# Kernel tuning notes

Measured on AMD Instinct MI355X. Metric: run time of the kernel, lower is better.

## Reference

```python
import jax, jax.numpy as jnp
import numpy as np

D_MODEL, N_HEADS, D_K, D_V = 1024, 16, 64, 64


def setup_inputs() -> dict:
    key = jax.random.key(0)
    ks = jax.random.split(key, 9)
    B, S = 8, 1024
    Q = jax.random.normal(ks[0], (B, S, D_MODEL), dtype=jnp.float32)
    K = jax.random.normal(ks[1], (B, S, D_MODEL), dtype=jnp.float32)
    V = jax.random.normal(ks[2], (B, S, D_MODEL), dtype=jnp.float32)
    # Xavier-uniform weights (gain=1): limit = sqrt(6/(fan_in+fan_out))
    lim = float(np.sqrt(6.0 / (D_MODEL + N_HEADS * D_K)))
    Wq = jax.random.uniform(ks[3], (D_MODEL, N_HEADS * D_K), minval=-lim, maxval=lim, dtype=jnp.float32)
    Wk = jax.random.uniform(ks[4], (D_MODEL, N_HEADS * D_K), minval=-lim, maxval=lim, dtype=jnp.float32)
    Wv = jax.random.uniform(ks[5], (D_MODEL, N_HEADS * D_V), minval=-lim, maxval=lim, dtype=jnp.float32)
    # nn.Linear default bias init: uniform(-1/sqrt(fan_in), 1/sqrt(fan_in))
    bl = float(1.0 / np.sqrt(D_MODEL))
    bq = jax.random.uniform(ks[6], (N_HEADS * D_K,), minval=-bl, maxval=bl, dtype=jnp.float32)
    bk = jax.random.uniform(ks[7], (N_HEADS * D_K,), minval=-bl, maxval=bl, dtype=jnp.float32)
    bv = jax.random.uniform(ks[8], (N_HEADS * D_V,), minval=-bl, maxval=bl, dtype=jnp.float32)
    return {"Q": Q, "K": K, "V": V, "Wq": Wq, "bq": bq, "Wk": Wk, "bk": bk, "Wv": Wv, "bv": bv}


def reference(Q, K, V, Wq, bq, Wk, bk, Wv, bv):
    B, S, _ = Q.shape
    # projections -> [B, H, S, d]
    q = (Q @ Wq + bq).reshape(B, S, N_HEADS, D_K).transpose(0, 2, 1, 3)
    k = (K @ Wk + bk).reshape(B, S, N_HEADS, D_K).transpose(0, 2, 1, 3)
    v = (V @ Wv + bv).reshape(B, S, N_HEADS, D_V).transpose(0, 2, 1, 3)
    scores = jnp.exp(jnp.einsum('bhqd,bhkd->bhqk', q, k) / jnp.sqrt(jnp.float32(D_K)))
    attn = scores / (jnp.sum(scores, axis=-1, keepdims=True) + 1e-8)
    ctx = jnp.einsum('bhqk,bhkd->bhqd', attn, v)  # [B,H,S,Dv]
    return ctx.transpose(0, 2, 1, 3).reshape(B, S, N_HEADS * D_V)
```

## Files before the change

### kernel.cpp

```cpp
#include <hip/hip_runtime.h>
#include <stdint.h>

#define DM 1024
#define HEADS 16
#define BATCH 8
#define SEQ 1024
#define MTOT 8192

typedef _Float16 half8 __attribute__((ext_vector_type(8)));
typedef _Float16 half4 __attribute__((ext_vector_type(4)));
typedef float floatx4 __attribute__((ext_vector_type(4)));

__device__ __forceinline__ void glds16(const void* g, void* l) {
    __builtin_amdgcn_global_load_lds(
        (const __attribute__((address_space(1))) void*)g,
        (__attribute__((address_space(3))) void*)l, 16, 0, 0);
}

__global__ __launch_bounds__(256) void cvt_inputs(
        const float* __restrict__ Q, const float* __restrict__ K,
        const float* __restrict__ V,
        _Float16* __restrict__ qb, _Float16* __restrict__ kb, _Float16* __restrict__ vb) {
    const float* src = blockIdx.y == 0 ? Q : (blockIdx.y == 1 ? K : V);
    _Float16* dst    = blockIdx.y == 0 ? qb : (blockIdx.y == 1 ? kb : vb);
    size_t i = ((size_t)blockIdx.x * 256 + threadIdx.x) * 8;
    float4 a = *(const float4*)(src + i);
    float4 b = *(const float4*)(src + i + 4);
    half8 h;
    h[0] = (_Float16)a.x; h[1] = (_Float16)a.y; h[2] = (_Float16)a.z; h[3] = (_Float16)a.w;
    h[4] = (_Float16)b.x; h[5] = (_Float16)b.y; h[6] = (_Float16)b.z; h[7] = (_Float16)b.w;
    *(half8*)(dst + i) = h;
}

__global__ __launch_bounds__(256) void cvt_w(
        const float* __restrict__ Wq, const float* __restrict__ Wk,
        const float* __restrict__ Wv,
        _Float16* __restrict__ wqt, _Float16* __restrict__ wkt, _Float16* __restrict__ wvt) {
    __shared__ float t[32][33];
    int z = blockIdx.z;
    const float* W = z == 0 ? Wq : (z == 1 ? Wk : Wv);
    _Float16* Wt   = z == 0 ? wqt : (z == 1 ? wkt : wvt);
    int k0 = blockIdx.x * 32, n0 = blockIdx.y * 32;
    int tx = threadIdx.x, ty = threadIdx.y;
#pragma unroll
    for (int i = 0; i < 4; i++)
        t[ty + i * 8][tx] = W[(size_t)(k0 + ty + i * 8) * DM + n0 + tx];
    __syncthreads();
#pragma unroll
    for (int i = 0; i < 4; i++)
        Wt[(size_t)(n0 + ty + i * 8) * DM + k0 + tx] = (_Float16)t[tx][ty + i * 8];
}

__global__ __launch_bounds__(256) void proj_gemm(
        const _Float16* __restrict__ qb, const _Float16* __restrict__ kb,
        const _Float16* __restrict__ vb,
        const _Float16* __restrict__ wqt, const _Float16* __restrict__ wkt,
        const _Float16* __restrict__ wvt,
        const float* __restrict__ bq, const float* __restrict__ bk,
        const float* __restrict__ bv,
        _Float16* __restrict__ qh, _Float16* __restrict__ kh, _Float16* __restrict__ vT) {
    __shared__ _Float16 As[128 * 64];
    __shared__ _Float16 Bs[128 * 64];
    int z = blockIdx.z;
    const _Float16* A  = z == 0 ? qb : (z == 1 ? kb : vb);
    const _Float16* Bw = z == 0 ? wqt : (z == 1 ? wkt : wvt);
    const float* bias  = z == 0 ? bq : (z == 1 ? bk : bv);
    int m0 = blockIdx.x * 128, n0 = blockIdx.y * 128;
    int tid = threadIdx.x, wid = tid >> 6, lane = tid & 63;
    int l15 = lane & 15, quad = lane >> 4;
    int wm = wid >> 1, wn = wid & 1;
    bool swapped = (z < 2);

    floatx4 acc[4][4] = {};

    for (int kb_ = 0; kb_ < 16; kb_++) {
        __syncthreads();
        int k0 = kb_ * 64;
        int r = (wid * 4) * 8 + (lane >> 3);
        int pg = (lane & 7) ^ (lane >> 3);
#pragma unroll
        for (int ii = 0; ii < 4; ii++) {
            int issue = wid * 4 + ii;
            int rr = r + ii * 8;
            glds16(A  + (size_t)(m0 + rr) * DM + k0 + pg * 8, &As[issue * 512]);
            glds16(Bw + (size_t)(n0 + rr) * DM + k0 + pg * 8, &Bs[issue * 512]);
        }
        __syncthreads();
#pragma unroll
        for (int kc = 0; kc < 2; kc++) {
            half8 a[4], b[4];
#pragma unroll
            for (int mt = 0; mt < 4; mt++) {
                int row = wm * 64 + mt * 16 + l15;
                int pl = (kc * 4 + quad) ^ (l15 & 7);
                a[mt] = *(const half8*)&As[row * 64 + pl * 8];
            }
#pragma unroll
            for (int nt = 0; nt < 4; nt++) {
                int row = wn * 64 + nt * 16 + l15;
                int pl = (kc * 4 + quad) ^ (l15 & 7);
                b[nt] = *(const half8*)&Bs[row * 64 + pl * 8];
            }
            if (swapped) {
#pragma unroll
                for (int mt = 0; mt < 4; mt++)
#pragma unroll
                    for (int nt = 0; nt < 4; nt++)
                        acc[mt][nt] = __builtin_amdgcn_mfma_f32_16x16x32_f16(
                            b[nt], a[mt], acc[mt][nt], 0, 0, 0);
            } else {
#pragma unroll
                for (int mt = 0; mt < 4; mt++)
#pragma unroll
                    for (int nt = 0; nt < 4; nt++)
                        acc[mt][nt] = __builtin_amdgcn_mfma_f32_16x16x32_f16(
                            a[mt], b[nt], acc[mt][nt], 0, 0, 0);
            }
        }
    }

    if (swapped) {
        float sc = (z == 0) ? 0.125f : 1.0f;
        _Float16* out = (z == 0) ? qh : kh;
#pragma unroll
        for (int nt = 0; nt < 4; nt++) {
            int d0 = n0 + wn * 64 + nt * 16 + quad * 4;
            int hh = d0 >> 6, dd = d0 & 63;
            floatx4 b4 = *(const floatx4*)&bias[d0];
#pragma unroll
            for (int mt = 0; mt < 4; mt++) {
                int s = m0 + wm * 64 + mt * 16 + l15;
                int b_ = s >> 10, ss = s & 1023;
                size_t off = ((size_t)(b_ * HEADS + hh)) * 65536 + (size_t)ss * 64 + dd;
                half4 hv;
#pragma unroll
                for (int r = 0; r < 4; r++)
                    hv[r] = (_Float16)((acc[mt][nt][r] + b4[r]) * sc);
                *(half4*)&out[off] = hv;
            }
        }
    } else {
#pragma unroll
        for (int nt = 0; nt < 4; nt++) {
            int d = n0 + wn * 64 + nt * 16 + l15;
            int hh = d >> 6, dd = d & 63;
            float bv_ = bias[d];
#pragma unroll
            for (int mt = 0; mt < 4; mt++) {
                int s0 = m0 + wm * 64 + mt * 16 + quad * 4;
                int b_ = s0 >> 10, ss = s0 & 1023;
                size_t off = ((size_t)(b_ * HEADS + hh)) * 65536 + (size_t)dd * 1024 + ss;
                half4 hv;
#pragma unroll
                for (int r = 0; r < 4; r++)
                    hv[r] = (_Float16)(acc[mt][nt][r] + bv_);
                *(half4*)&vT[off] = hv;
            }
        }
    }
}

__global__ __launch_bounds__(256) void attn(
        const _Float16* __restrict__ qh, const _Float16* __restrict__ kh,
        const _Float16* __restrict__ vT, float* __restrict__ out) {
    __shared__ _Float16 Ks[4096];
    __shared__ _Float16 Vs[4096];
    __shared__ _Float16 QP[16384];
    int qt = blockIdx.x, h = blockIdx.y, b = blockIdx.z;
    size_t base = ((size_t)(b * HEADS + h)) * 65536;
    int tid = threadIdx.x, wid = tid >> 6, lane = tid & 63;
    int l15 = lane & 15, quad = lane >> 4;
    int rs = lane >> 3;
    int pg = (lane & 7) ^ rs;

#pragma unroll
    for (int ii = 0; ii < 8; ii++) {
        int issue = wid * 8 + ii;
        int r = issue * 8 + rs;
        glds16(qh + base + (size_t)(qt * 256 + r) * 64 + pg * 8, &QP[issue * 512]);
    }
    __syncthreads();
    half8 qf[4][2];
#pragma unroll
    for (int mt = 0; mt < 4; mt++)
#pragma unroll
        for (int kc = 0; kc < 2; kc++) {
            int row = wid * 64 + mt * 16 + l15;
            int pl = (kc * 4 + quad) ^ (l15 & 7);
            qf[mt][kc] = *(const half8*)&QP[row * 64 + pl * 8];
        }
    __syncthreads();

    floatx4 oacc[4][4] = {};
    float rden[4] = {0.f, 0.f, 0.f, 0.f};
    _Float16* Pw = &QP[wid * 4096];

    for (int kt = 0; kt < 16; kt++) {
        __syncthreads();
#pragma unroll
        for (int ii = 0; ii < 2; ii++) {
            int issue = wid * 2 + ii;
            int r = issue * 8 + rs;
            glds16(kh + base + (size_t)(kt * 64 + r) * 64 + pg * 8, &Ks[issue * 512]);
            glds16(vT + base + (size_t)r * 1024 + kt * 64 + pg * 8, &Vs[issue * 512]);
        }
        __syncthreads();

#pragma unroll
        for (int hf = 0; hf < 2; hf++) {
            floatx4 sacc[2][4] = {};
#pragma unroll
            for (int kc = 0; kc < 2; kc++) {
                half8 kf[2];
#pragma unroll
                for (int kn2 = 0; kn2 < 2; kn2++) {
                    int kn = hf * 2 + kn2;
                    int pl = (kc * 4 + quad) ^ (l15 & 7);
                    kf[kn2] = *(const half8*)&Ks[(kn * 16 + l15) * 64 + pl * 8];
                }
#pragma unroll
                for (int kn2 = 0; kn2 < 2; kn2++)
#pragma unroll
                    for (int mt = 0; mt < 4; mt++)
                        sacc[kn2][mt] = __builtin_amdgcn_mfma_f32_16x16x32_f16(
                            kf[kn2], qf[mt][kc], sacc[kn2][mt], 0, 0, 0);
            }
#pragma unroll
            for (int kn2 = 0; kn2 < 2; kn2++) {
                int kn = hf * 2 + kn2;
#pragma unroll
                for (int mt = 0; mt < 4; mt++) {
                    half4 ph;
#pragma unroll
                    for (int r = 0; r < 4; r++) {
                        float p = __expf(sacc[kn2][mt][r]);
                        rden[mt] += p;
                        ph[r] = (_Float16)p;
                    }
                    *(half4*)&Pw[(kn * 2 + (quad >> 1)) * 512 + (mt * 16 + l15) * 8 +
                                 (quad & 1) * 4] = ph;
                }
            }
            half8 af[4], vf[4];
#pragma unroll
            for (int mt = 0; mt < 4; mt++)
                af[mt] = *(const half8*)&Pw[(hf * 4 + quad) * 512 + (mt * 16 + l15) * 8];
#pragma unroll
            for (int dn = 0; dn < 4; dn++) {
                int pl = (hf * 4 + quad) ^ (l15 & 7);
                vf[dn] = *(const half8*)&Vs[(dn * 16 + l15) * 64 + pl * 8];
            }
#pragma unroll
            for (int mt = 0; mt < 4; mt++)
#pragma unroll
                for (int dn = 0; dn < 4; dn++)
                    oacc[mt][dn] = __builtin_amdgcn_mfma_f32_16x16x32_f16(
                        af[mt], vf[dn], oacc[mt][dn], 0, 0, 0);
        }
    }

#pragma unroll
    for (int mt = 0; mt < 4; mt++) {
        float d = rden[mt];
        d += __shfl_xor(d, 16, 64);
        d += __shfl_xor(d, 32, 64);
        rden[mt] = 1.0f / (d + 1e-8f);
    }
#pragma unroll
    for (int mt = 0; mt < 4; mt++) {
#pragma unroll
        for (int r = 0; r < 4; r++) {
            float dinv = __shfl(rden[mt], quad * 4 + r, 16);
            int s = qt * 256 + wid * 64 + mt * 16 + quad * 4 + r;
#pragma unroll
            for (int dn = 0; dn < 4; dn++) {
                int col = h * 64 + dn * 16 + l15;
                out[((size_t)(b * SEQ + s)) * 1024 + col] = oacc[mt][dn][r] * dinv;
            }
        }
    }
}

extern "C" void kernel_launch(void* const* d_in, const int* in_sizes, int n_in,
                              void* d_out, int out_size, void* d_ws, size_t ws_size,
                              hipStream_t stream) {
    const float* Q  = (const float*)d_in[0];
    const float* K  = (const float*)d_in[1];
    const float* V  = (const float*)d_in[2];
    const float* Wq = (const float*)d_in[3];
    const float* bq = (const float*)d_in[4];
    const float* Wk = (const float*)d_in[5];
    const float* bk = (const float*)d_in[6];
    const float* Wv = (const float*)d_in[7];
    const float* bv = (const float*)d_in[8];
    float* out = (float*)d_out;

    char* ws = (char*)d_ws;
    const size_t TEN = (size_t)MTOT * DM * sizeof(_Float16);
    _Float16* qb  = (_Float16*)(ws);
    _Float16* kb  = (_Float16*)(ws + TEN);
    _Float16* vb  = (_Float16*)(ws + 2 * TEN);
    _Float16* qh  = (_Float16*)(ws + 3 * TEN);
    _Float16* kh  = (_Float16*)(ws + 4 * TEN);
    _Float16* vT  = (_Float16*)(ws + 5 * TEN);
    const size_t WTN = (size_t)DM * DM * sizeof(_Float16);
    _Float16* wqt = (_Float16*)(ws + 6 * TEN);
    _Float16* wkt = (_Float16*)(ws + 6 * TEN + WTN);
    _Float16* wvt = (_Float16*)(ws + 6 * TEN + 2 * WTN);

    cvt_inputs<<<dim3(4096, 3), 256, 0, stream>>>(Q, K, V, qb, kb, vb);
    cvt_w<<<dim3(32, 32, 3), dim3(32, 8), 0, stream>>>(Wq, Wk, Wv, wqt, wkt, wvt);
    proj_gemm<<<dim3(64, 8, 3), 256, 0, stream>>>(qb, kb, vb, wqt, wkt, wvt,
                                                  bq, bk, bv, qh, kh, vT);
    attn<<<dim3(4, 16, 8), 256, 0, stream>>>(qh, kh, vT, out);
}
```

Measured before the change: 285.0 us.

## Fuse fp32-to-fp16 input conversion into projection GEMM with double-buffered LDS

Removes the separate cvt_inputs kernel and makes proj_gemm load fp32 Q/K/V directly, convert them in registers and store fp16 into LDS. It also double-buffers the A and B LDS tiles so the loads for the next k-block overlap the MFMAs on the current one. This saves a full fp32 read plus fp16 write and re-read of the three input tensors, and one launch. In exchange the GEMM reads twice as many A bytes from global memory through registers instead of direct-to-LDS loads, and uses more LDS and registers, which may lower occupancy.

```diff
diff --git a/kernel.cpp b/kernel.cpp
--- a/kernel.cpp
+++ b/kernel.cpp
@@ -15,21 +15,6 @@
     __builtin_amdgcn_global_load_lds(
         (const __attribute__((address_space(1))) void*)g,
         (__attribute__((address_space(3))) void*)l, 16, 0, 0);
-}
-
-__global__ __launch_bounds__(256) void cvt_inputs(
-        const float* __restrict__ Q, const float* __restrict__ K,
-        const float* __restrict__ V,
-        _Float16* __restrict__ qb, _Float16* __restrict__ kb, _Float16* __restrict__ vb) {
-    const float* src = blockIdx.y == 0 ? Q : (blockIdx.y == 1 ? K : V);
-    _Float16* dst    = blockIdx.y == 0 ? qb : (blockIdx.y == 1 ? kb : vb);
-    size_t i = ((size_t)blockIdx.x * 256 + threadIdx.x) * 8;
-    float4 a = *(const float4*)(src + i);
-    float4 b = *(const float4*)(src + i + 4);
-    half8 h;
-    h[0] = (_Float16)a.x; h[1] = (_Float16)a.y; h[2] = (_Float16)a.z; h[3] = (_Float16)a.w;
-    h[4] = (_Float16)b.x; h[5] = (_Float16)b.y; h[6] = (_Float16)b.z; h[7] = (_Float16)b.w;
-    *(half8*)(dst + i) = h;
 }
 
 __global__ __launch_bounds__(256) void cvt_w(
@@ -52,17 +37,17 @@
 }
 
 __global__ __launch_bounds__(256) void proj_gemm(
-        const _Float16* __restrict__ qb, const _Float16* __restrict__ kb,
-        const _Float16* __restrict__ vb,
+        const float* __restrict__ Qf, const float* __restrict__ Kf,
+        const float* __restrict__ Vf,
         const _Float16* __restrict__ wqt, const _Float16* __restrict__ wkt,
         const _Float16* __restrict__ wvt,
         const float* __restrict__ bq, const float* __restrict__ bk,
         const float* __restrict__ bv,
         _Float16* __restrict__ qh, _Float16* __restrict__ kh, _Float16* __restrict__ vT) {
-    __shared__ _Float16 As[128 * 64];
-    __shared__ _Float16 Bs[128 * 64];
+    __shared__ _Float16 As[2][128 * 64];
+    __shared__ _Float16 Bs[2][128 * 64];
     int z = blockIdx.z;
-    const _Float16* A  = z == 0 ? qb : (z == 1 ? kb : vb);
+    const float* A     = z == 0 ? Qf : (z == 1 ? Kf : Vf);
     const _Float16* Bw = z == 0 ? wqt : (z == 1 ? wkt : wvt);
     const float* bias  = z == 0 ? bq : (z == 1 ? bk : bv);
     int m0 = blockIdx.x * 128, n0 = blockIdx.y * 128;
@@ -71,21 +56,47 @@
     int wm = wid >> 1, wn = wid & 1;
     bool swapped = (z < 2);
 
+    int rbase = wid * 32 + (lane >> 3);
+    int pg = (lane & 7) ^ (lane >> 3);
+
     floatx4 acc[4][4] = {};
+    float4 a0[4], a1[4];
+
+#pragma unroll
+    for (int ii = 0; ii < 4; ii++) {
+        int rr = rbase + ii * 8;
+        const float* src = A + (size_t)(m0 + rr) * DM + pg * 8;
+        a0[ii] = *(const float4*)src;
+        a1[ii] = *(const float4*)(src + 4);
+        glds16(Bw + (size_t)(n0 + rr) * DM + pg * 8, &Bs[0][(wid * 4 + ii) * 512]);
+    }
+#pragma unroll
+    for (int ii = 0; ii < 4; ii++) {
+        half8 h;
+        h[0] = (_Float16)a0[ii].x; h[1] = (_Float16)a0[ii].y;
+        h[2] = (_Float16)a0[ii].z; h[3] = (_Float16)a0[ii].w;
+        h[4] = (_Float16)a1[ii].x; h[5] = (_Float16)a1[ii].y;
+        h[6] = (_Float16)a1[ii].z; h[7] = (_Float16)a1[ii].w;
+        *(half8*)&As[0][(wid * 4 + ii) * 512 + lane * 8] = h;
+    }
+    __syncthreads();
 
     for (int kb_ = 0; kb_ < 16; kb_++) {
-        __syncthreads();
-        int k0 = kb_ * 64;
-        int r = (wid * 4) * 8 + (lane >> 3);
-        int pg = (lane & 7) ^ (lane >> 3);
-#pragma unroll
-        for (int ii = 0; ii < 4; ii++) {
-            int issue = wid * 4 + ii;
-            int rr = r + ii * 8;
-            glds16(A  + (size_t)(m0 + rr) * DM + k0 + pg * 8, &As[issue * 512]);
-            glds16(Bw + (size_t)(n0 + rr) * DM + k0 + pg * 8, &Bs[issue * 512]);
-        }
-        __syncthreads();
+        int cur = kb_ & 1;
+
+        if (kb_ < 15) {
+            int k0 = (kb_ + 1) * 64;
+#pragma unroll
+            for (int ii = 0; ii < 4; ii++) {
+                int rr = rbase + ii * 8;
+                const float* src = A + (size_t)(m0 + rr) * DM + k0 + pg * 8;
+                a0[ii] = *(const float4*)src;
+                a1[ii] = *(const float4*)(src + 4);
+                glds16(Bw + (size_t)(n0 + rr) * DM + k0 + pg * 8,
+                       &Bs[cur ^ 1][(wid * 4 + ii) * 512]);
+            }
+        }
+
 #pragma unroll
         for (int kc = 0; kc < 2; kc++) {
             half8 a[4], b[4];
@@ -93,13 +104,13 @@
             for (int mt = 0; mt < 4; mt++) {
                 int row = wm * 64 + mt * 16 + l15;
                 int pl = (kc * 4 + quad) ^ (l15 & 7);
-                a[mt] = *(const half8*)&As[row * 64 + pl * 8];
+                a[mt] = *(const half8*)&As[cur][row * 64 + pl * 8];
             }
 #pragma unroll
             for (int nt = 0; nt < 4; nt++) {
                 int row = wn * 64 + nt * 16 + l15;
                 int pl = (kc * 4 + quad) ^ (l15 & 7);
-                b[nt] = *(const half8*)&Bs[row * 64 + pl * 8];
+                b[nt] = *(const half8*)&Bs[cur][row * 64 + pl * 8];
             }
             if (swapped) {
 #pragma unroll
@@ -117,6 +128,19 @@
                             a[mt], b[nt], acc[mt][nt], 0, 0, 0);
             }
         }
+
+        if (kb_ < 15) {
+#pragma unroll
+            for (int ii = 0; ii < 4; ii++) {
+                half8 h;
+                h[0] = (_Float16)a0[ii].x; h[1] = (_Float16)a0[ii].y;
+                h[2] = (_Float16)a0[ii].z; h[3] = (_Float16)a0[ii].w;
+                h[4] = (_Float16)a1[ii].x; h[5] = (_Float16)a1[ii].y;
+                h[6] = (_Float16)a1[ii].z; h[7] = (_Float16)a1[ii].w;
+                *(half8*)&As[cur ^ 1][(wid * 4 + ii) * 512 + lane * 8] = h;
+            }
+        }
+        __syncthreads();
     }
 
     if (swapped) {
@@ -297,20 +321,16 @@
 
     char* ws = (char*)d_ws;
     const size_t TEN = (size_t)MTOT * DM * sizeof(_Float16);
-    _Float16* qb  = (_Float16*)(ws);
-    _Float16* kb  = (_Float16*)(ws + TEN);
-    _Float16* vb  = (_Float16*)(ws + 2 * TEN);
-    _Float16* qh  = (_Float16*)(ws + 3 * TEN);
-    _Float16* kh  = (_Float16*)(ws + 4 * TEN);
-    _Float16* vT  = (_Float16*)(ws + 5 * TEN);
+    _Float16* qh  = (_Float16*)(ws);
+    _Float16* kh  = (_Float16*)(ws + TEN);
+    _Float16* vT  = (_Float16*)(ws + 2 * TEN);
     const size_t WTN = (size_t)DM * DM * sizeof(_Float16);
-    _Float16* wqt = (_Float16*)(ws + 6 * TEN);
-    _Float16* wkt = (_Float16*)(ws + 6 * TEN + WTN);
-    _Float16* wvt = (_Float16*)(ws + 6 * TEN + 2 * WTN);
-
-    cvt_inputs<<<dim3(4096, 3), 256, 0, stream>>>(Q, K, V, qb, kb, vb);
+    _Float16* wqt = (_Float16*)(ws + 3 * TEN);
+    _Float16* wkt = (_Float16*)(ws + 3 * TEN + WTN);
+    _Float16* wvt = (_Float16*)(ws + 3 * TEN + 2 * WTN);
+
     cvt_w<<<dim3(32, 32, 3), dim3(32, 8), 0, stream>>>(Wq, Wk, Wv, wqt, wkt, wvt);
-    proj_gemm<<<dim3(64, 8, 3), 256, 0, stream>>>(qb, kb, vb, wqt, wkt, wvt,
+    proj_gemm<<<dim3(64, 8, 3), 256, 0, stream>>>(Q, K, V, wqt, wkt, wvt,
                                                   bq, bk, bv, qh, kh, vT);
     attn<<<dim3(4, 16, 8), 256, 0, stream>>>(qh, kh, vT, out);
 }
```

After: 299.0 us. 4.9% more time.
